# Performance work log

Hardware: AMD Instinct MI355X
Metric: run time of the kernel (lower is better)

## Reference

```python
import jax, jax.numpy as jnp
import numpy as np


def setup_inputs() -> dict:
    key = jax.random.key(0)
    inp = jax.random.normal(key, (8, 3, 224, 224), dtype=jnp.float32)
    return {"inp": inp, "tau_min": 1, "tau_max": 60, "ntau": 8,
            "num_angles": 12, "stride": 2}


def _logpolar_offsets(tau_min, tau_max, ntau, num_angles):
    # Matches the torch module: theta in [-pi, pi), tau logarithmically spaced,
    # coords stacked angle-major as (y, x) pairs (theta unsqueeze(1) outer).
    c = (tau_max / tau_min) ** (1.0 / (ntau - 1)) - 1.0
    theta = np.arange(num_angles, dtype=np.float64) * (2.0 * np.pi / num_angles) - np.pi
    tau = tau_min * (1.0 + c) ** np.arange(ntau, dtype=np.float64)
    x = tau[None, :] * np.cos(theta[:, None])   # (A, T)
    y = tau[None, :] * np.sin(theta[:, None])   # (A, T)
    return (jnp.asarray(y.ravel(), jnp.float32),
            jnp.asarray(x.ravel(), jnp.float32))  # each (A*T,)


def reference(inp, tau_min, tau_max, ntau, num_angles, stride):
    yoff, xoff = _logpolar_offsets(tau_min, tau_max, ntau, num_angles)
    B, F, H, W = inp.shape
    Hs = (H - 1) // stride + 1
    Ws = (W - 1) // stride + 1
    gy = jnp.arange(Hs, dtype=jnp.float32) * stride   # focus-point rows
    gx = jnp.arange(Ws, dtype=jnp.float32) * stride   # focus-point cols

    def sample(yo, xo):
        # Bilinear sample of inp at (i*stride + yo, j*stride + xo), zero outside.
        yq = gy + yo
        xq = gx + xo
        y0 = jnp.floor(yq)
        x0 = jnp.floor(xq)
        wy = (yq - y0)  # (Hs,)
        wx = (xq - x0)  # (Ws,)
        y0i = y0.astype(jnp.int32)
        x0i = x0.astype(jnp.int32)

        def gather(yi, xi):
            vy = ((yi >= 0) & (yi < H)).astype(inp.dtype)
            vx = ((xi >= 0) & (xi < W)).astype(inp.dtype)
            g = inp[:, :, jnp.clip(yi, 0, H - 1), :][:, :, :, jnp.clip(xi, 0, W - 1)]
            return g * (vy[:, None] * vx[None, :])  # (B,F,Hs,Ws)

        w00 = (1 - wy)[:, None] * (1 - wx)[None, :]
        w01 = (1 - wy)[:, None] * wx[None, :]
        w10 = wy[:, None] * (1 - wx)[None, :]
        w11 = wy[:, None] * wx[None, :]
        return (w00 * gather(y0i, x0i) + w01 * gather(y0i, x0i + 1)
                + w10 * gather(y0i + 1, x0i) + w11 * gather(y0i + 1, x0i + 1))

    out = jax.vmap(sample)(yoff, xoff)                    # (A*T, B, F, Hs, Ws)
    out = out.reshape(num_angles, ntau, B, F, Hs, Ws)
    out = jnp.transpose(out, (2, 3, 1, 0, 4, 5))          # (B, F, ntau, A, Hs, Ws)
    return out
```

## Files before the change

kernel.cpp:

```cpp
#include <hip/hip_runtime.h>
#include <cmath>
#include <algorithm>

#ifndef M_PI
#define M_PI 3.14159265358979323846
#endif

#define B_ 8
#define F_ 3
#define H_ 224
#define W_ 224
#define T_ 8
#define A_ 12
#define NK 96
#define HS_ 112
#define WS_ 112
#define PLANE_ (H_ * W_)
#define SLICE_ (HS_ * WS_)

#define RI 8
#define BANDROWS 78
#define PH 57
#define PITCH 228
#define NLANE 56

struct LPArgs {
    int   cy[NK];  int cx[NK];
    float fy[NK];  float fx[NK];
    int   korig[NK];
    int   cymin[2]; int cymax[2];
};

static LPArgs make_args() {
    int cy[NK], cx[NK]; float fy[NK], fx[NK];
    double c = pow(60.0, 1.0 / 7.0) - 1.0;
    for (int t = 0; t < T_; ++t) {
        double tau = pow(1.0 + c, (double)t);
        for (int a = 0; a < A_; ++a) {
            double th = (double)a * (2.0 * M_PI / (double)A_) - M_PI;
            float yo = (float)(tau * sin(th)), xo = (float)(tau * cos(th));
            int k = t * A_ + a;
            float yf = floorf(yo), xf = floorf(xo);
            cy[k] = (int)yf; fy[k] = yo - yf;
            cx[k] = (int)xf; fx[k] = xo - xf;
        }
    }
    int idx[NK];
    for (int k = 0; k < NK; ++k) idx[k] = k;
    std::sort(idx, idx + NK, [&](int a, int b) { return cy[a] < cy[b]; });
    LPArgs r;
    r.cymin[0] = r.cymin[1] = 1000; r.cymax[0] = r.cymax[1] = -1000;
    for (int p = 0; p < NK; ++p) {
        int k = idx[p], g = p / 48;
        r.cy[p] = cy[k]; r.cx[p] = cx[k];
        r.fy[p] = fy[k]; r.fx[p] = fx[k];
        r.korig[p] = k;
        r.cymin[g] = std::min(r.cymin[g], cy[k]);
        r.cymax[g] = std::max(r.cymax[g], cy[k]);
    }
    return r;
}

__global__ __launch_bounds__(1024, 8) void lp_sample_kernel(
    const float* __restrict__ inp, float* __restrict__ out, LPArgs args) {

    __shared__ float lds[BANDROWS * PITCH];

    const int bf = blockIdx.x;
    const int i0 = blockIdx.y * RI;
    const int g  = blockIdx.z;

    const int r0 = max(0, 2 * i0 + args.cymin[g]);
    const int r1 = min(H_ - 1, 2 * i0 + 2 * (RI - 1) + args.cymax[g] + 1);
    const int nrows = min(r1 - r0 + 1, BANDROWS);

    const float* plane = inp + (size_t)bf * PLANE_;

    {
        const int n = nrows * (W_ / 4);
        for (int v = threadIdx.x; v < n; v += 1024) {
            const unsigned r = (unsigned)v / 56u;
            const int u = v - (int)r * 56;
            const float4 val = *(const float4*)(plane + (size_t)(r0 + (int)r) * W_ + 4 * u);
            float* rowp = lds + r * PITCH + u;
            rowp[0 * PH] = val.x;
            rowp[1 * PH] = val.y;
            rowp[2 * PH] = val.z;
            rowp[3 * PH] = val.w;
        }
    }
    __syncthreads();

    const int lane = threadIdx.x & 63;
    const int wave = __builtin_amdgcn_readfirstlane((int)threadIdx.x >> 6);

    float* outp = out + (size_t)bf * (NK * SLICE_) + (size_t)i0 * WS_;
    const bool act = (lane < NLANE);

#pragma unroll 1
    for (int tt = 0; tt < 3; ++tt) {
        const int kk = g * 48 + wave + (tt << 4);

        const int   cy = args.cy[kk]; const float fy = args.fy[kk];
        const int   cx = args.cx[kk]; const float fx = args.fx[kk];
        const int   ko = args.korig[kk];
        const float omfx = 1.0f - fx;

        const int l = lane;
        const float* tp[4];
        float tw[4];
#pragma unroll
        for (int t = 0; t < 4; ++t) {
            const int s   = cx + t;
            const int ct  = 4 * l + s;
            const int ph  = s & 3;
            int idx = l + (s >> 2);
            idx = min(max(idx, 0), NLANE - 1);
            tp[t] = lds + ph * PH + idx;
            const float wbase = (t & 1) ? fx : omfx;
            tw[t] = (ct >= 0 && ct < W_) ? wbase : 0.0f;
        }

        float2* orow = (float2*)(outp + (size_t)ko * SLICE_) + l;

        if (act) {
#pragma unroll 2
            for (int di = 0; di < RI; ++di) {
                const int iy0 = 2 * (i0 + di) + cy;
                float mA, mB;
                if (iy0 >= 0 && iy0 <= H_ - 2)  { mA = 1.0f - fy; mB = fy; }
                else if (iy0 == -1)             { mA = fy;        mB = 0.0f; }
                else if (iy0 == H_ - 1)         { mA = 0.0f;      mB = 1.0f - fy; }
                else                            { mA = 0.0f;      mB = 0.0f; }
                const int by = min(max(iy0, 0), H_ - 2);
                const int rb = min(by - r0, BANDROWS - 2) * PITCH;

                const float a0 = tp[0][rb], a1 = tp[0][rb + PITCH];
                const float b0 = tp[1][rb], b1 = tp[1][rb + PITCH];
                const float c0 = tp[2][rb], c1 = tp[2][rb + PITCH];
                const float d0 = tp[3][rb], d1 = tp[3][rb + PITCH];

                float2 rr;
                rr.x = mA * (tw[0] * a0 + tw[1] * b0)
                     + mB * (tw[0] * a1 + tw[1] * b1);
                rr.y = mA * (tw[2] * c0 + tw[3] * d0)
                     + mB * (tw[2] * c1 + tw[3] * d1);

                orow[(size_t)di * (WS_ / 2)] = rr;
            }
        }
    }
}

extern "C" void kernel_launch(void* const* d_in, const int* in_sizes, int n_in,
                              void* d_out, int out_size, void* d_ws, size_t ws_size,
                              hipStream_t stream) {
    const float* inp = (const float*)d_in[0];
    float*       out = (float*)d_out;

    static const LPArgs args = make_args();

    lp_sample_kernel<<<dim3(B_ * F_, HS_ / RI, 2), 1024, 0, stream>>>(inp, out, args);
}
```

Measured before the change: 133.9 us.

## Pre-permute input into phase layout and stage it with async global-to-LDS copies

Adds a separate kernel that rewrites the input into a phase-split row layout in workspace memory. The main kernel can then copy band rows straight into LDS with global_load_lds async copies instead of scattering float4 components through registers. The cost is an extra launch and a full read and write of the input. The LDS pitch also changes from 57 to 56 per phase, which may add bank conflicts. The old kernel is kept as a fallback when no workspace is provided.

```diff
diff --git a/kernel.cpp b/kernel.cpp
--- a/kernel.cpp
+++ b/kernel.cpp
@@ -1,6 +1,7 @@
 #include <hip/hip_runtime.h>
 #include <cmath>
 #include <algorithm>
+#include <cstdint>
 
 #ifndef M_PI
 #define M_PI 3.14159265358979323846
@@ -20,9 +21,9 @@
 
 #define RI 8
 #define BANDROWS 78
-#define PH 57
-#define PITCH 228
 #define NLANE 56
+#define PH4 56
+#define PITCH4 224
 
 struct LPArgs {
     int   cy[NK];  int cx[NK];
@@ -61,10 +62,29 @@
     return r;
 }
 
-__global__ __launch_bounds__(1024, 8) void lp_sample_kernel(
-    const float* __restrict__ inp, float* __restrict__ out, LPArgs args) {
-
-    __shared__ float lds[BANDROWS * PITCH];
+typedef __attribute__((address_space(3))) unsigned int       lds_u32;
+typedef __attribute__((address_space(1))) const unsigned int glb_u32;
+static __device__ __forceinline__ void async_copy16(const void* g, void* l) {
+    __builtin_amdgcn_global_load_lds((glb_u32*)g, (lds_u32*)l, 16, 0, 0);
+}
+
+__global__ __launch_bounds__(256) void lp_permute_kernel(
+    const float* __restrict__ inp, float* __restrict__ P) {
+    const int q = (int)blockIdx.x * 256 + (int)threadIdx.x;
+    const float4 v = ((const float4*)inp)[q];
+    const int bfr = q / PH4;
+    const int u   = q - bfr * PH4;
+    float* row = P + (size_t)bfr * PITCH4;
+    row[u]           = v.x;
+    row[PH4 + u]     = v.y;
+    row[2 * PH4 + u] = v.z;
+    row[3 * PH4 + u] = v.w;
+}
+
+__global__ __launch_bounds__(1024, 8) void lp_main_kernel(
+    const float* __restrict__ P, float* __restrict__ out, LPArgs args) {
+
+    __shared__ float lds[BANDROWS * PITCH4];
 
     const int bf = blockIdx.x;
     const int i0 = blockIdx.y * RI;
@@ -74,25 +94,18 @@
     const int r1 = min(H_ - 1, 2 * i0 + 2 * (RI - 1) + args.cymax[g] + 1);
     const int nrows = min(r1 - r0 + 1, BANDROWS);
 
-    const float* plane = inp + (size_t)bf * PLANE_;
-
-    {
-        const int n = nrows * (W_ / 4);
-        for (int v = threadIdx.x; v < n; v += 1024) {
-            const unsigned r = (unsigned)v / 56u;
-            const int u = v - (int)r * 56;
-            const float4 val = *(const float4*)(plane + (size_t)(r0 + (int)r) * W_ + 4 * u);
-            float* rowp = lds + r * PITCH + u;
-            rowp[0 * PH] = val.x;
-            rowp[1 * PH] = val.y;
-            rowp[2 * PH] = val.z;
-            rowp[3 * PH] = val.w;
-        }
-    }
-    __syncthreads();
-
     const int lane = threadIdx.x & 63;
     const int wave = __builtin_amdgcn_readfirstlane((int)threadIdx.x >> 6);
+
+    const float* src = P + (size_t)bf * PLANE_ + (size_t)r0 * PITCH4;
+    const int Db = nrows * (PITCH4 * 4);
+    const int C  = Db >> 10;
+    for (int c = wave; c < C; c += 16)
+        async_copy16(src + c * 256 + lane * 4, (char*)lds + (c << 10));
+    const int tail4 = (Db - (C << 10)) >> 4;
+    for (int t = threadIdx.x; t < tail4; t += 1024)
+        ((float4*)lds)[(C << 6) + t] = ((const float4*)src)[(C << 6) + t];
+    __syncthreads();
 
     float* outp = out + (size_t)bf * (NK * SLICE_) + (size_t)i0 * WS_;
     const bool act = (lane < NLANE);
@@ -111,14 +124,13 @@
         float tw[4];
 #pragma unroll
         for (int t = 0; t < 4; ++t) {
-            const int s   = cx + t;
-            const int ct  = 4 * l + s;
-            const int ph  = s & 3;
+            const int s  = cx + t;
+            const int ct = 4 * l + s;
+            const int ph = s & 3;
             int idx = l + (s >> 2);
-            idx = min(max(idx, 0), NLANE - 1);
-            tp[t] = lds + ph * PH + idx;
-            const float wbase = (t & 1) ? fx : omfx;
-            tw[t] = (ct >= 0 && ct < W_) ? wbase : 0.0f;
+            idx = min(max(idx, 0), PH4 - 1);
+            tp[t] = lds + ph * PH4 + idx;
+            tw[t] = (ct >= 0 && ct < W_) ? ((t & 1) ? fx : omfx) : 0.0f;
         }
 
         float2* orow = (float2*)(outp + (size_t)ko * SLICE_) + l;
@@ -133,12 +145,12 @@
                 else if (iy0 == H_ - 1)         { mA = 0.0f;      mB = 1.0f - fy; }
                 else                            { mA = 0.0f;      mB = 0.0f; }
                 const int by = min(max(iy0, 0), H_ - 2);
-                const int rb = min(by - r0, BANDROWS - 2) * PITCH;
-
-                const float a0 = tp[0][rb], a1 = tp[0][rb + PITCH];
-                const float b0 = tp[1][rb], b1 = tp[1][rb + PITCH];
-                const float c0 = tp[2][rb], c1 = tp[2][rb + PITCH];
-                const float d0 = tp[3][rb], d1 = tp[3][rb + PITCH];
+                const int rb = min(by - r0, BANDROWS - 2) * PITCH4;
+
+                const float a0 = tp[0][rb], a1 = tp[0][rb + PITCH4];
+                const float b0 = tp[1][rb], b1 = tp[1][rb + PITCH4];
+                const float c0 = tp[2][rb], c1 = tp[2][rb + PITCH4];
+                const float d0 = tp[3][rb], d1 = tp[3][rb + PITCH4];
 
                 float2 rr;
                 rr.x = mA * (tw[0] * a0 + tw[1] * b0)
@@ -152,6 +164,82 @@
     }
 }
 
+#define FPH 57
+#define FPITCH 228
+__global__ __launch_bounds__(1024, 8) void lp_fallback_kernel(
+    const float* __restrict__ inp, float* __restrict__ out, LPArgs args) {
+
+    __shared__ float lds[BANDROWS * FPITCH];
+
+    const int bf = blockIdx.x;
+    const int i0 = blockIdx.y * RI;
+    const int g  = blockIdx.z;
+
+    const int r0 = max(0, 2 * i0 + args.cymin[g]);
+    const int r1 = min(H_ - 1, 2 * i0 + 2 * (RI - 1) + args.cymax[g] + 1);
+    const int nrows = min(r1 - r0 + 1, BANDROWS);
+
+    const float* plane = inp + (size_t)bf * PLANE_;
+    {
+        const int n = nrows * (W_ / 4);
+        for (int v = threadIdx.x; v < n; v += 1024) {
+            const unsigned r = (unsigned)v / 56u;
+            const int u = v - (int)r * 56;
+            const float4 val = *(const float4*)(plane + (size_t)(r0 + (int)r) * W_ + 4 * u);
+            float* rowp = lds + r * FPITCH + u;
+            rowp[0 * FPH] = val.x; rowp[1 * FPH] = val.y;
+            rowp[2 * FPH] = val.z; rowp[3 * FPH] = val.w;
+        }
+    }
+    __syncthreads();
+
+    const int lane = threadIdx.x & 63;
+    const int wave = __builtin_amdgcn_readfirstlane((int)threadIdx.x >> 6);
+    float* outp = out + (size_t)bf * (NK * SLICE_) + (size_t)i0 * WS_;
+    const bool act = (lane < NLANE);
+
+#pragma unroll 1
+    for (int tt = 0; tt < 3; ++tt) {
+        const int kk = g * 48 + wave + (tt << 4);
+        const int   cy = args.cy[kk]; const float fy = args.fy[kk];
+        const int   cx = args.cx[kk]; const float fx = args.fx[kk];
+        const int   ko = args.korig[kk];
+        const float omfx = 1.0f - fx;
+        const int l = lane;
+        const float* tp[4]; float tw[4];
+#pragma unroll
+        for (int t = 0; t < 4; ++t) {
+            const int s = cx + t; const int ct = 4 * l + s; const int ph = s & 3;
+            int idx = l + (s >> 2);
+            idx = min(max(idx, 0), NLANE - 1);
+            tp[t] = lds + ph * FPH + idx;
+            tw[t] = (ct >= 0 && ct < W_) ? ((t & 1) ? fx : omfx) : 0.0f;
+        }
+        float2* orow = (float2*)(outp + (size_t)ko * SLICE_) + l;
+        if (act) {
+#pragma unroll 2
+            for (int di = 0; di < RI; ++di) {
+                const int iy0 = 2 * (i0 + di) + cy;
+                float mA, mB;
+                if (iy0 >= 0 && iy0 <= H_ - 2)  { mA = 1.0f - fy; mB = fy; }
+                else if (iy0 == -1)             { mA = fy;        mB = 0.0f; }
+                else if (iy0 == H_ - 1)         { mA = 0.0f;      mB = 1.0f - fy; }
+                else                            { mA = 0.0f;      mB = 0.0f; }
+                const int by = min(max(iy0, 0), H_ - 2);
+                const int rb = min(by - r0, BANDROWS - 2) * FPITCH;
+                const float a0 = tp[0][rb], a1 = tp[0][rb + FPITCH];
+                const float b0 = tp[1][rb], b1 = tp[1][rb + FPITCH];
+                const float c0 = tp[2][rb], c1 = tp[2][rb + FPITCH];
+                const float d0 = tp[3][rb], d1 = tp[3][rb + FPITCH];
+                float2 rr;
+                rr.x = mA * (tw[0] * a0 + tw[1] * b0) + mB * (tw[0] * a1 + tw[1] * b1);
+                rr.y = mA * (tw[2] * c0 + tw[3] * d0) + mB * (tw[2] * c1 + tw[3] * d1);
+                orow[(size_t)di * (WS_ / 2)] = rr;
+            }
+        }
+    }
+}
+
 extern "C" void kernel_launch(void* const* d_in, const int* in_sizes, int n_in,
                               void* d_out, int out_size, void* d_ws, size_t ws_size,
                               hipStream_t stream) {
@@ -160,5 +248,12 @@
 
     static const LPArgs args = make_args();
 
-    lp_sample_kernel<<<dim3(B_ * F_, HS_ / RI, 2), 1024, 0, stream>>>(inp, out, args);
-}
+    const size_t needP = (size_t)B_ * F_ * PLANE_ * sizeof(float);
+    if (d_ws != nullptr && ws_size >= needP) {
+        float* P = (float*)d_ws;
+        lp_permute_kernel<<<dim3((B_ * F_ * PLANE_ / 4) / 256), 256, 0, stream>>>(inp, P);
+        lp_main_kernel<<<dim3(B_ * F_, HS_ / RI, 2), 1024, 0, stream>>>(P, out, args);
+    } else {
+        lp_fallback_kernel<<<dim3(B_ * F_, HS_ / RI, 2), 1024, 0, stream>>>(inp, out, args);
+    }
+}
```

Result: no change. 136.4 us (+1.9%).
